# Kernel tuning notes

Hardware: AMD Instinct MI355X
Metric: run time of the kernel (lower is better)

## Reference

```python
import jax, jax.numpy as jnp
import numpy as np
import math

B, T, C = 8, 1024, 64  # n_head = 1 (forced by the module's relative-attention matmul shapes)


def setup_inputs() -> dict:
    key = jax.random.key(0)
    ks = jax.random.split(key, 7)
    x = jax.random.normal(ks[0], (B, T, C), dtype=jnp.float32)
    Wqkv = jax.random.normal(ks[1], (3 * C, C), dtype=jnp.float32) * 0.02
    bqkv = jnp.zeros((3 * C,), dtype=jnp.float32)
    embk = jax.random.normal(ks[2], (T, C), dtype=jnp.float32) * 0.02
    embv = jax.random.normal(ks[3], (T, C), dtype=jnp.float32) * 0.02
    Wproj = jax.random.normal(ks[4], (C, C), dtype=jnp.float32) * 0.02
    bproj = jnp.zeros((C,), dtype=jnp.float32)
    return {"x": x, "Wqkv": Wqkv, "bqkv": bqkv, "embk": embk, "embv": embv,
            "Wproj": Wproj, "bproj": bproj}


def reference(x, Wqkv, bqkv, embk, embv, Wproj, bproj):
    b, t, c = x.shape
    qkv = x @ Wqkv.T + bqkv                      # [B,T,3C]
    q, k, v = jnp.split(qkv, 3, axis=2)          # each [B,T,C]; n_head=1 so head_dim=C

    # relative_pos[i,j] = (i-j).tril() -> 0 above diagonal (masked out anyway)
    idx = jnp.arange(t)
    rel = jnp.tril(idx[:, None] - idx[None, :])  # [T,T] ints in [0, T-1]
    rk = embk[rel]                               # [T,T,C] gathered relative keys
    rv = embv[rel]                               # [T,T,C] gathered relative values

    att1 = jnp.einsum('btc,bsc->bts', q, k)      # content-content scores
    att2 = jnp.einsum('tbc,tsc->bts', q.transpose(1, 0, 2), rk)  # content-position scores
    scale = 1.0 / math.sqrt(c)
    att = (att1 + att2) * scale

    causal = jnp.tril(jnp.ones((t, t), dtype=bool))
    att = jnp.where(causal[None, :, :], att, -jnp.inf)
    att = jax.nn.softmax(att, axis=-1)           # [B,T,T]

    y1 = jnp.einsum('bts,bsc->btc', att, v)      # content values
    y2 = jnp.einsum('bts,tsc->btc', att, rv)     # relative values
    y = y1 + y2                                  # [B,T,C]
    return y @ Wproj.T + bproj
```

## Files before the change

kernel.cpp:

```cpp
#include <hip/hip_runtime.h>
#include <math.h>

#define BB 8
#define TT 1024
#define CC 64

typedef float f32x4 __attribute__((ext_vector_type(4)));
typedef short short8 __attribute__((ext_vector_type(8)));
typedef unsigned int u32x4 __attribute__((ext_vector_type(4)));
typedef unsigned short u16;

static __device__ __forceinline__ u16 f2bf(float f) {
    union { float f; unsigned int u; } v; v.f = f;
    unsigned int r = v.u + 0x7fffu + ((v.u >> 16) & 1u);
    return (u16)(r >> 16);
}
static __device__ __forceinline__ float bf2f(u16 h) {
    union { unsigned int u; float f; } v; v.u = ((unsigned int)h) << 16; return v.f;
}
static __device__ __forceinline__ short8 pack8(const float* p) {
    float4 a = *(const float4*)p;
    float4 b = *(const float4*)(p + 4);
    short8 r;
    r[0] = (short)f2bf(a.x); r[1] = (short)f2bf(a.y); r[2] = (short)f2bf(a.z); r[3] = (short)f2bf(a.w);
    r[4] = (short)f2bf(b.x); r[5] = (short)f2bf(b.y); r[6] = (short)f2bf(b.z); r[7] = (short)f2bf(b.w);
    return r;
}

#define MFMA16(a, b, c) __builtin_amdgcn_mfma_f32_16x16x32_bf16((a), (b), (c), 0, 0, 0)

#define OFF_QBF      ((size_t)0)
#define OFF_KBF      ((size_t)1048576)
#define OFF_VT       ((size_t)2097152)
#define OFF_EKP      ((size_t)3145728)
#define OFF_EVT      ((size_t)3284992)
#define OFF_WPROJ    ((size_t)3424256)
#define OFF_YP       ((size_t)3432448)
#define OFF_LP       ((size_t)20209664)
#define WS_NEED      ((size_t)20471808)

__global__ __launch_bounds__(256) void qkv_prep_kernel(const float* __restrict__ x,
                                                       const float* __restrict__ Wqkv,
                                                       const float* __restrict__ bqkv,
                                                       const float* __restrict__ embk,
                                                       const float* __restrict__ embv,
                                                       const float* __restrict__ Wproj,
                                                       u16* __restrict__ q_bf,
                                                       u16* __restrict__ k_bf,
                                                       u16* __restrict__ vT_bf,
                                                       u16* __restrict__ embk_pad,
                                                       u16* __restrict__ embvT_pad,
                                                       u16* __restrict__ Wproj_bf) {
    const int blk = blockIdx.x;
    const int grp = blockIdx.y;
    const int tid = threadIdx.x;

    if (blk >= 512) {
        if (grp != 0) return;
        const int idx0 = (blk - 512) * 256 + tid;
        const int stride = 64 * 256;
        for (int i = idx0; i < 1088 * CC; i += stride) {
            int r = i >> 6, c = i & 63, d = r - 32;
            embk_pad[i] = (d >= 0 && d < TT) ? f2bf(embk[d * CC + c]) : (u16)0;
        }
        for (int i = idx0; i < CC * 1088; i += stride) {
            int c = i / 1088, col = i - c * 1088, d = col - 32;
            embvT_pad[i] = (d >= 0 && d < TT) ? f2bf(embv[d * CC + c]) : (u16)0;
        }
        for (int i = idx0; i < CC * CC; i += stride) Wproj_bf[i] = f2bf(Wproj[i]);
        return;
    }

    const int w = tid >> 6, lane = tid & 63, quad = lane >> 4, l15 = lane & 15;
    const int row0 = blk * 16;
    const int oc = grp * 4 + w;
    __shared__ float vt[4][16][17];

    const float* xr = x + (size_t)(row0 + l15) * CC + quad * 8;
    short8 a0 = pack8(xr);
    short8 a1 = pack8(xr + 32);

    const float* wr = Wqkv + (size_t)(oc * 16 + l15) * CC + quad * 8;
    short8 b0 = pack8(wr);
    short8 b1 = pack8(wr + 32);
    f32x4 acc = {0.f, 0.f, 0.f, 0.f};
    acc = MFMA16(a0, b0, acc);
    acc = MFMA16(a1, b1, acc);
    const float bias = bqkv[oc * 16 + l15];

    if (oc < 4) {
        const int c = oc * 16 + l15;
        #pragma unroll
        for (int r = 0; r < 4; ++r)
            q_bf[(size_t)(row0 + quad * 4 + r) * CC + c] = f2bf((acc[r] + bias) * 0.125f);
    } else if (oc < 8) {
        const int c = (oc - 4) * 16 + l15;
        #pragma unroll
        for (int r = 0; r < 4; ++r)
            k_bf[(size_t)(row0 + quad * 4 + r) * CC + c] = f2bf(acc[r] + bias);
    } else {
        #pragma unroll
        for (int r = 0; r < 4; ++r) vt[w][quad * 4 + r][l15] = acc[r] + bias;
        const int c_l = lane >> 2;
        const int tbase = (lane & 3) * 4;
        const int b = row0 >> 10, t0v = row0 & (TT - 1);
        u16 p[4];
        #pragma unroll
        for (int tt2 = 0; tt2 < 4; ++tt2) p[tt2] = f2bf(vt[w][tbase + tt2][c_l]);
        unsigned long long pk = (unsigned long long)p[0] | ((unsigned long long)p[1] << 16)
                              | ((unsigned long long)p[2] << 32) | ((unsigned long long)p[3] << 48);
        *(unsigned long long*)&vT_bf[(size_t)(b * CC + (oc - 8) * 16 + c_l) * TT + t0v + tbase] = pk;
    }
}

#define WBSTRIDE 4160

__global__ __launch_bounds__(256) void attn_part_kernel(const u16* __restrict__ q_bf,
                                                        const u16* __restrict__ k_bf,
                                                        const u16* __restrict__ vT_bf,
                                                        const u16* __restrict__ embk_pad,
                                                        const u16* __restrict__ embvT_pad,
                                                        float* __restrict__ Ypart,
                                                        float* __restrict__ Lpart) {
    const int b = blockIdx.y;
    int xx = blockIdx.x;
    int tt = 0, slot = 0;
    for (tt = 0; tt < 64; ++tt) {
        const int c = ((tt >> 1) + 4) >> 2;
        if (xx < c) { slot = xx; break; }
        xx -= c;
    }
    const int t0 = tt * 16;
    const int nst = (t0 >> 5) + 1;

    const int tid = threadIdx.x;
    const int w = tid >> 6, lane = tid & 63, quad = lane >> 4, l15 = lane & 15;
    const int st = slot * 4 + w;
    const bool active = (st < nst);

    __shared__ __align__(16) char wbuf[4][WBSTRIDE];
    __shared__ float lpart[4][16];

    u16* pt = (u16*)(wbuf[w]);
    u16* a2 = (u16*)(wbuf[w] + 1280);

    f32x4 acc[4];
    #pragma unroll
    for (int nb = 0; nb < 4; ++nb) acc[nb] = (f32x4){0.f, 0.f, 0.f, 0.f};
    float rsum[4] = {0.f, 0.f, 0.f, 0.f};

    if (active) {
        const int s0 = st * 32;

        const u16* qrow = q_bf + (size_t)((b << 10) + t0 + l15) * CC;
        short8 aq0 = *(const short8*)(qrow + quad * 8);
        short8 aq1 = *(const short8*)(qrow + 32 + quad * 8);

        f32x4 sc[2];
        #pragma unroll
        for (int cb = 0; cb < 2; ++cb) {
            const u16* krow = k_bf + (size_t)((b << 10) + s0 + cb * 16 + l15) * CC;
            short8 kb0 = *(const short8*)(krow + quad * 8);
            short8 kb1 = *(const short8*)(krow + 32 + quad * 8);
            f32x4 a = {0.f, 0.f, 0.f, 0.f};
            a = MFMA16(aq0, kb0, a);
            a = MFMA16(aq1, kb1, a);
            sc[cb] = a;
        }

        const int dbase = t0 - s0 - 31;
        f32x4 bnd[3];
        #pragma unroll
        for (int nb = 0; nb < 3; ++nb) {
            const u16* erow = embk_pad + (size_t)(dbase + 32 + nb * 16 + l15) * CC;
            short8 eb0 = *(const short8*)(erow + quad * 8);
            short8 eb1 = *(const short8*)(erow + 32 + quad * 8);
            f32x4 a = {0.f, 0.f, 0.f, 0.f};
            a = MFMA16(aq0, eb0, a);
            a = MFMA16(aq1, eb1, a);
            bnd[nb] = a;
        }

        u16 pb0[4], pb1[4];
        #pragma unroll
        for (int r = 0; r < 4; ++r) {
            const int i = quad * 4 + r;
            const int u0 = 31 + i - l15;
            const int src = (quad << 4) | (u0 & 15);
            const float v0 = __shfl(bnd[0][r], src, 64);
            const float v1 = __shfl(bnd[1][r], src, 64);
            const float v2 = __shfl(bnd[2][r], src, 64);
            const bool hi = (u0 >= 32);
            {
                const float rb = hi ? v2 : v1;
                const int d = t0 - s0 + i - l15;
                float pv = (d >= 0) ? __expf(sc[0][r] + rb) : 0.f;
                pb0[r] = f2bf(pv);
                rsum[r] += bf2f(pb0[r]);
            }
            {
                const float rb = hi ? v1 : v0;
                const int d = t0 - s0 + i - 16 - l15;
                float pv = (d >= 0) ? __expf(sc[1][r] + rb) : 0.f;
                pb1[r] = f2bf(pv);
                rsum[r] += bf2f(pb1[r]);
            }
        }

        u32x4 z = {0u, 0u, 0u, 0u};
        #pragma unroll
        for (int e = 0; e < 3; ++e) {
            int idx = lane + e * 64;
            if (idx < 144) ((u32x4*)a2)[idx] = z;
        }
        #pragma unroll
        for (int r = 0; r < 4; ++r) {
            const int i = quad * 4 + r;
            pt[i * 40 + l15] = pb0[r];
            pt[i * 40 + 16 + l15] = pb1[r];
            a2[i * 72 + (32 + i - l15)] = pb0[r];
            a2[i * 72 + (16 + i - l15)] = pb1[r];
        }

        short8 aP = *(const short8*)(pt + l15 * 40 + quad * 8);
        #pragma unroll
        for (int nb = 0; nb < 4; ++nb) {
            const u16* vrow = vT_bf + ((size_t)(b * CC + nb * 16 + l15) << 10) + s0;
            short8 bv = *(const short8*)(vrow + quad * 8);
            acc[nb] = MFMA16(aP, bv, acc[nb]);
        }

        const int dcol0 = t0 - s0;
        #pragma unroll
        for (int kk = 0; kk < 2; ++kk) {
            short8 a2f = *(const short8*)(a2 + l15 * 72 + kk * 32 + quad * 8);
            #pragma unroll
            for (int nb = 0; nb < 4; ++nb) {
                const u16* erow = embvT_pad + (size_t)(nb * 16 + l15) * 1088 + dcol0 + kk * 32 + quad * 8;
                short8 be = *(const short8*)erow;
                acc[nb] = MFMA16(a2f, be, acc[nb]);
            }
        }
    }

    #pragma unroll
    for (int msk = 1; msk < 16; msk <<= 1)
        #pragma unroll
        for (int r = 0; r < 4; ++r) rsum[r] += __shfl_xor(rsum[r], msk, 64);
    if (l15 == 0) {
        #pragma unroll
        for (int r = 0; r < 4; ++r) lpart[w][quad * 4 + r] = rsum[r];
    }

    float* ypw = (float*)(wbuf[w]);
    #pragma unroll
    for (int nb = 0; nb < 4; ++nb)
        #pragma unroll
        for (int r = 0; r < 4; ++r)
            ypw[(quad * 4 + r) * 64 + nb * 16 + l15] = acc[nb][r];
    __syncthreads();

    const size_t sbase = ((size_t)((b * 64 + tt) * 8 + slot)) << 10;
    {
        const int i = tid >> 4, c0 = (tid * 4) & 63;
        float4 Y;
        Y.x = ((float*)(wbuf[0]))[i * 64 + c0]     + ((float*)(wbuf[1]))[i * 64 + c0]
            + ((float*)(wbuf[2]))[i * 64 + c0]     + ((float*)(wbuf[3]))[i * 64 + c0];
        Y.y = ((float*)(wbuf[0]))[i * 64 + c0 + 1] + ((float*)(wbuf[1]))[i * 64 + c0 + 1]
            + ((float*)(wbuf[2]))[i * 64 + c0 + 1] + ((float*)(wbuf[3]))[i * 64 + c0 + 1];
        Y.z = ((float*)(wbuf[0]))[i * 64 + c0 + 2] + ((float*)(wbuf[1]))[i * 64 + c0 + 2]
            + ((float*)(wbuf[2]))[i * 64 + c0 + 2] + ((float*)(wbuf[3]))[i * 64 + c0 + 2];
        Y.w = ((float*)(wbuf[0]))[i * 64 + c0 + 3] + ((float*)(wbuf[1]))[i * 64 + c0 + 3]
            + ((float*)(wbuf[2]))[i * 64 + c0 + 3] + ((float*)(wbuf[3]))[i * 64 + c0 + 3];
        *(float4*)&Ypart[sbase + (size_t)tid * 4] = Y;
    }
    if (tid < 16)
        Lpart[((size_t)((b * 64 + tt) * 8 + slot)) * 16 + tid] =
            lpart[0][tid] + lpart[1][tid] + lpart[2][tid] + lpart[3][tid];
}

__global__ __launch_bounds__(256) void norm_proj_kernel(const float* __restrict__ Ypart,
                                                        const float* __restrict__ Lpart,
                                                        const u16* __restrict__ Wproj_bf,
                                                        const float* __restrict__ bproj,
                                                        float* __restrict__ out) {
    const int b = blockIdx.y;
    const int tt = blockIdx.x;
    const int t0 = tt * 16;
    const int nslots = ((tt >> 1) + 4) >> 2;
    const int tid = threadIdx.x;
    const int w = tid >> 6, lane = tid & 63, quad = lane >> 4, l15 = lane & 15;

    __shared__ float Ls[16];
    __shared__ __align__(16) u16 yA[16 * 64];

    const size_t base = ((size_t)((b * 64 + tt) * 8)) << 10;
    float4 Y = {0.f, 0.f, 0.f, 0.f};
    for (int s = 0; s < nslots; ++s) {
        float4 v = *(const float4*)&Ypart[base + ((size_t)s << 10) + (size_t)tid * 4];
        Y.x += v.x; Y.y += v.y; Y.z += v.z; Y.w += v.w;
    }
    if (tid < 16) {
        float L = 0.f;
        for (int s = 0; s < nslots; ++s)
            L += Lpart[((size_t)((b * 64 + tt) * 8 + s)) * 16 + tid];
        Ls[tid] = L;
    }
    __syncthreads();

    const int i = tid >> 4, c0 = (tid * 4) & 63;
    const float inv = 1.0f / Ls[i];
    u16 y4[4] = { f2bf(Y.x * inv), f2bf(Y.y * inv), f2bf(Y.z * inv), f2bf(Y.w * inv) };
    *(unsigned long long*)&yA[i * 64 + c0] =
        (unsigned long long)y4[0] | ((unsigned long long)y4[1] << 16)
      | ((unsigned long long)y4[2] << 32) | ((unsigned long long)y4[3] << 48);
    __syncthreads();

    short8 a0 = *(const short8*)(yA + l15 * 64 + quad * 8);
    short8 a1 = *(const short8*)(yA + l15 * 64 + 32 + quad * 8);
    const u16* wrow = Wproj_bf + (size_t)(w * 16 + l15) * CC;
    short8 wb0 = *(const short8*)(wrow + quad * 8);
    short8 wb1 = *(const short8*)(wrow + 32 + quad * 8);
    f32x4 o = {0.f, 0.f, 0.f, 0.f};
    o = MFMA16(a0, wb0, o);
    o = MFMA16(a1, wb1, o);
    const float bias = bproj[w * 16 + l15];
    #pragma unroll
    for (int r = 0; r < 4; ++r)
        out[(size_t)((b << 10) + t0 + quad * 4 + r) * CC + w * 16 + l15] = o[r] + bias;
}

__global__ __launch_bounds__(192) void qkv_kernel(const float* __restrict__ x,
                                                  const float* __restrict__ Wqkv,
                                                  const float* __restrict__ bqkv,
                                                  float* __restrict__ qkv) {
    __shared__ __align__(16) float xs[CC];
    const int row = blockIdx.x;
    const int j = threadIdx.x;
    if (j < CC) xs[j] = x[row * CC + j];
    __syncthreads();
    const float* w = Wqkv + j * CC;
    float acc = bqkv[j];
    #pragma unroll
    for (int c = 0; c < CC; c += 4) {
        float4 wq = *(const float4*)(w + c);
        float4 xq = *(const float4*)(xs + c);
        acc += wq.x * xq.x + wq.y * xq.y + wq.z * xq.z + wq.w * xq.w;
    }
    qkv[row * 192 + j] = acc;
}

__global__ __launch_bounds__(256) void attn_kernel(const float* __restrict__ qkv,
                                                   const float* __restrict__ embk,
                                                   const float* __restrict__ embv,
                                                   const float* __restrict__ Wproj,
                                                   const float* __restrict__ bproj,
                                                   float* __restrict__ out) {
    __shared__ __align__(16) float qs[CC];
    __shared__ __align__(16) float sc[TT];
    __shared__ float red[256];
    __shared__ float yred[4][CC];
    const int bt = blockIdx.x;
    const int b = bt >> 10, t = bt & (TT - 1);
    const int tid = threadIdx.x;
    if (tid < CC) qs[tid] = qkv[bt * 192 + tid];
    __syncthreads();
    float lmax = -1e30f;
    for (int s = tid; s <= t; s += 256) {
        const float* krow = qkv + (b * TT + s) * 192 + 64;
        const float* erow = embk + (t - s) * CC;
        float acc = 0.f;
        #pragma unroll
        for (int c = 0; c < CC; c += 4) {
            float4 kq = *(const float4*)(krow + c);
            float4 eq = *(const float4*)(erow + c);
            float4 qq = *(const float4*)(qs + c);
            acc += qq.x * (kq.x + eq.x) + qq.y * (kq.y + eq.y)
                 + qq.z * (kq.z + eq.z) + qq.w * (kq.w + eq.w);
        }
        acc *= 0.125f;
        sc[s] = acc;
        lmax = fmaxf(lmax, acc);
    }
    red[tid] = lmax; __syncthreads();
    for (int off = 128; off > 0; off >>= 1) { if (tid < off) red[tid] = fmaxf(red[tid], red[tid + off]); __syncthreads(); }
    const float m = red[0]; __syncthreads();
    float lsum = 0.f;
    for (int s = tid; s <= t; s += 256) { float e = __expf(sc[s] - m); sc[s] = e; lsum += e; }
    red[tid] = lsum; __syncthreads();
    for (int off = 128; off > 0; off >>= 1) { if (tid < off) red[tid] += red[tid + off]; __syncthreads(); }
    const float inv = 1.0f / red[0]; __syncthreads();
    const int c = tid & 63, g = tid >> 6;
    float acc = 0.f;
    for (int s = g; s <= t; s += 4) {
        float p = sc[s];
        float vv = qkv[(b * TT + s) * 192 + 128 + c];
        float ev = embv[(t - s) * CC + c];
        acc += p * (vv + ev);
    }
    yred[g][c] = acc * inv;
    __syncthreads();
    if (tid < CC) qs[tid] = yred[0][tid] + yred[1][tid] + yred[2][tid] + yred[3][tid];
    __syncthreads();
    if (tid < CC) {
        const float* w = Wproj + tid * CC;
        float o = bproj[tid];
        #pragma unroll
        for (int cc2 = 0; cc2 < CC; cc2 += 4) {
            float4 wq = *(const float4*)(w + cc2);
            float4 yq = *(const float4*)(qs + cc2);
            o += wq.x * yq.x + wq.y * yq.y + wq.z * yq.z + wq.w * yq.w;
        }
        out[bt * CC + tid] = o;
    }
}

extern "C" void kernel_launch(void* const* d_in, const int* in_sizes, int n_in,
                              void* d_out, int out_size, void* d_ws, size_t ws_size,
                              hipStream_t stream) {
    const float* x     = (const float*)d_in[0];
    const float* Wqkv  = (const float*)d_in[1];
    const float* bqkv  = (const float*)d_in[2];
    const float* embk  = (const float*)d_in[3];
    const float* embv  = (const float*)d_in[4];
    const float* Wproj = (const float*)d_in[5];
    const float* bproj = (const float*)d_in[6];
    float* out = (float*)d_out;

    if (ws_size < WS_NEED) {
        float* qkv = (float*)d_ws;
        qkv_kernel<<<BB * TT, 192, 0, stream>>>(x, Wqkv, bqkv, qkv);
        attn_kernel<<<BB * TT, 256, 0, stream>>>(qkv, embk, embv, Wproj, bproj, out);
        return;
    }

    char* ws = (char*)d_ws;
    u16* q_bf       = (u16*)(ws + OFF_QBF);
    u16* k_bf       = (u16*)(ws + OFF_KBF);
    u16* vT_bf      = (u16*)(ws + OFF_VT);
    u16* embk_pad   = (u16*)(ws + OFF_EKP);
    u16* embvT_pad  = (u16*)(ws + OFF_EVT);
    u16* Wproj_bf   = (u16*)(ws + OFF_WPROJ);
    float* Ypart    = (float*)(ws + OFF_YP);
    float* Lpart    = (float*)(ws + OFF_LP);

    qkv_prep_kernel<<<dim3(576, 3), 256, 0, stream>>>(x, Wqkv, bqkv, embk, embv, Wproj,
                                                      q_bf, k_bf, vT_bf, embk_pad, embvT_pad, Wproj_bf);
    attn_part_kernel<<<dim3(288, 8), 256, 0, stream>>>(q_bf, k_bf, vT_bf, embk_pad, embvT_pad,
                                                       Ypart, Lpart);
    norm_proj_kernel<<<dim3(64, 8), 256, 0, stream>>>(Ypart, Lpart, Wproj_bf, bproj, out);
}
```

Baseline: 111.0 us.

## Fuse split-K reduction and output projection into attention kernel via last-block counter

Removes the separate normalize/projection kernel. Each attention block writes its partial result, then bumps a per-tile atomic counter, and the last block to finish reduces all partials and applies the output projection. Tiles with a single slot skip the global partial writes entirely. Counters are zeroed in the prep kernel. This saves one kernel launch and some global traffic, at the cost of threadfences, atomics and a serialized tail on the last block.

New measurement: 419.3 us. +277.8%, slower.

```diff
diff --git a/kernel.cpp b/kernel.cpp
--- a/kernel.cpp
+++ b/kernel.cpp
@@ -37,7 +37,8 @@
 #define OFF_WPROJ    ((size_t)3424256)
 #define OFF_YP       ((size_t)3432448)
 #define OFF_LP       ((size_t)20209664)
-#define WS_NEED      ((size_t)20471808)
+#define OFF_CNT      ((size_t)20471808)
+#define WS_NEED      ((size_t)20473856)
 
 __global__ __launch_bounds__(256) void qkv_prep_kernel(const float* __restrict__ x,
                                                        const float* __restrict__ Wqkv,
@@ -50,12 +51,18 @@
                                                        u16* __restrict__ vT_bf,
                                                        u16* __restrict__ embk_pad,
                                                        u16* __restrict__ embvT_pad,
-                                                       u16* __restrict__ Wproj_bf) {
+                                                       u16* __restrict__ Wproj_bf,
+                                                       int* __restrict__ cnt) {
     const int blk = blockIdx.x;
     const int grp = blockIdx.y;
     const int tid = threadIdx.x;
 
     if (blk >= 512) {
+        if (grp == 1) {
+            const int idx = (blk - 512) * 256 + tid;
+            if (idx < BB * 64) cnt[idx] = 0;
+            return;
+        }
         if (grp != 0) return;
         const int idx0 = (blk - 512) * 256 + tid;
         const int stride = 64 * 256;
@@ -115,13 +122,17 @@
 
 #define WBSTRIDE 4160
 
-__global__ __launch_bounds__(256) void attn_part_kernel(const u16* __restrict__ q_bf,
-                                                        const u16* __restrict__ k_bf,
-                                                        const u16* __restrict__ vT_bf,
-                                                        const u16* __restrict__ embk_pad,
-                                                        const u16* __restrict__ embvT_pad,
-                                                        float* __restrict__ Ypart,
-                                                        float* __restrict__ Lpart) {
+__global__ __launch_bounds__(256) void attn_fused_kernel(const u16* __restrict__ q_bf,
+                                                         const u16* __restrict__ k_bf,
+                                                         const u16* __restrict__ vT_bf,
+                                                         const u16* __restrict__ embk_pad,
+                                                         const u16* __restrict__ embvT_pad,
+                                                         float* __restrict__ Ypart,
+                                                         float* __restrict__ Lpart,
+                                                         const u16* __restrict__ Wproj_bf,
+                                                         const float* __restrict__ bproj,
+                                                         float* __restrict__ out,
+                                                         int* __restrict__ cnt) {
     const int b = blockIdx.y;
     int xx = blockIdx.x;
     int tt = 0, slot = 0;
@@ -132,6 +143,7 @@
     }
     const int t0 = tt * 16;
     const int nst = (t0 >> 5) + 1;
+    const int nslots = ((tt >> 1) + 4) >> 2;
 
     const int tid = threadIdx.x;
     const int w = tid >> 6, lane = tid & 63, quad = lane >> 4, l15 = lane & 15;
@@ -140,6 +152,9 @@
 
     __shared__ __align__(16) char wbuf[4][WBSTRIDE];
     __shared__ float lpart[4][16];
+    __shared__ float Ls[16];
+    __shared__ __align__(16) u16 yA[16 * 64];
+    __shared__ int isLast;
 
     u16* pt = (u16*)(wbuf[w]);
     u16* a2 = (u16*)(wbuf[w] + 1280);
@@ -260,55 +275,52 @@
             ypw[(quad * 4 + r) * 64 + nb * 16 + l15] = acc[nb][r];
     __syncthreads();
 
-    const size_t sbase = ((size_t)((b * 64 + tt) * 8 + slot)) << 10;
-    {
-        const int i = tid >> 4, c0 = (tid * 4) & 63;
-        float4 Y;
-        Y.x = ((float*)(wbuf[0]))[i * 64 + c0]     + ((float*)(wbuf[1]))[i * 64 + c0]
-            + ((float*)(wbuf[2]))[i * 64 + c0]     + ((float*)(wbuf[3]))[i * 64 + c0];
-        Y.y = ((float*)(wbuf[0]))[i * 64 + c0 + 1] + ((float*)(wbuf[1]))[i * 64 + c0 + 1]
-            + ((float*)(wbuf[2]))[i * 64 + c0 + 1] + ((float*)(wbuf[3]))[i * 64 + c0 + 1];
-        Y.z = ((float*)(wbuf[0]))[i * 64 + c0 + 2] + ((float*)(wbuf[1]))[i * 64 + c0 + 2]
-            + ((float*)(wbuf[2]))[i * 64 + c0 + 2] + ((float*)(wbuf[3]))[i * 64 + c0 + 2];
-        Y.w = ((float*)(wbuf[0]))[i * 64 + c0 + 3] + ((float*)(wbuf[1]))[i * 64 + c0 + 3]
-            + ((float*)(wbuf[2]))[i * 64 + c0 + 3] + ((float*)(wbuf[3]))[i * 64 + c0 + 3];
+    const int i = tid >> 4, c0 = (tid * 4) & 63;
+    float4 Y;
+    Y.x = ((float*)(wbuf[0]))[i * 64 + c0]     + ((float*)(wbuf[1]))[i * 64 + c0]
+        + ((float*)(wbuf[2]))[i * 64 + c0]     + ((float*)(wbuf[3]))[i * 64 + c0];
+    Y.y = ((float*)(wbuf[0]))[i * 64 + c0 + 1] + ((float*)(wbuf[1]))[i * 64 + c0 + 1]
+        + ((float*)(wbuf[2]))[i * 64 + c0 + 1] + ((float*)(wbuf[3]))[i * 64 + c0 + 1];
+    Y.z = ((float*)(wbuf[0]))[i * 64 + c0 + 2] + ((float*)(wbuf[1]))[i * 64 + c0 + 2]
+        + ((float*)(wbuf[2]))[i * 64 + c0 + 2] + ((float*)(wbuf[3]))[i * 64 + c0 + 2];
+    Y.w = ((float*)(wbuf[0]))[i * 64 + c0 + 3] + ((float*)(wbuf[1]))[i * 64 + c0 + 3]
+        + ((float*)(wbuf[2]))[i * 64 + c0 + 3] + ((float*)(wbuf[3]))[i * 64 + c0 + 3];
+
+    if (nslots > 1) {
+        const size_t sbase = ((size_t)((b * 64 + tt) * 8 + slot)) << 10;
         *(float4*)&Ypart[sbase + (size_t)tid * 4] = Y;
-    }
-    if (tid < 16)
-        Lpart[((size_t)((b * 64 + tt) * 8 + slot)) * 16 + tid] =
-            lpart[0][tid] + lpart[1][tid] + lpart[2][tid] + lpart[3][tid];
-}
-
-__global__ __launch_bounds__(256) void norm_proj_kernel(const float* __restrict__ Ypart,
-                                                        const float* __restrict__ Lpart,
-                                                        const u16* __restrict__ Wproj_bf,
-                                                        const float* __restrict__ bproj,
-                                                        float* __restrict__ out) {
-    const int b = blockIdx.y;
-    const int tt = blockIdx.x;
-    const int t0 = tt * 16;
-    const int nslots = ((tt >> 1) + 4) >> 2;
-    const int tid = threadIdx.x;
-    const int w = tid >> 6, lane = tid & 63, quad = lane >> 4, l15 = lane & 15;
-
-    __shared__ float Ls[16];
-    __shared__ __align__(16) u16 yA[16 * 64];
-
-    const size_t base = ((size_t)((b * 64 + tt) * 8)) << 10;
-    float4 Y = {0.f, 0.f, 0.f, 0.f};
-    for (int s = 0; s < nslots; ++s) {
-        float4 v = *(const float4*)&Ypart[base + ((size_t)s << 10) + (size_t)tid * 4];
-        Y.x += v.x; Y.y += v.y; Y.z += v.z; Y.w += v.w;
-    }
-    if (tid < 16) {
-        float L = 0.f;
-        for (int s = 0; s < nslots; ++s)
-            L += Lpart[((size_t)((b * 64 + tt) * 8 + s)) * 16 + tid];
-        Ls[tid] = L;
-    }
-    __syncthreads();
-
-    const int i = tid >> 4, c0 = (tid * 4) & 63;
+        if (tid < 16)
+            Lpart[((size_t)((b * 64 + tt) * 8 + slot)) * 16 + tid] =
+                lpart[0][tid] + lpart[1][tid] + lpart[2][tid] + lpart[3][tid];
+        __threadfence();
+        if (tid == 0) {
+            const int old = atomicAdd(&cnt[b * 64 + tt], 1);
+            isLast = (old == nslots - 1);
+        }
+        __syncthreads();
+        if (!isLast) return;
+        __threadfence();
+
+        const size_t base = ((size_t)((b * 64 + tt) * 8)) << 10;
+        for (int s = 0; s < nslots; ++s) {
+            if (s == slot) continue;
+            float4 v = *(const float4*)&Ypart[base + ((size_t)s << 10) + (size_t)tid * 4];
+            Y.x += v.x; Y.y += v.y; Y.z += v.z; Y.w += v.w;
+        }
+        if (tid < 16) {
+            float L = lpart[0][tid] + lpart[1][tid] + lpart[2][tid] + lpart[3][tid];
+            for (int s = 0; s < nslots; ++s) {
+                if (s == slot) continue;
+                L += Lpart[((size_t)((b * 64 + tt) * 8 + s)) * 16 + tid];
+            }
+            Ls[tid] = L;
+        }
+    } else {
+        if (tid < 16)
+            Ls[tid] = lpart[0][tid] + lpart[1][tid] + lpart[2][tid] + lpart[3][tid];
+    }
+    __syncthreads();
+
     const float inv = 1.0f / Ls[i];
     u16 y4[4] = { f2bf(Y.x * inv), f2bf(Y.y * inv), f2bf(Y.z * inv), f2bf(Y.w * inv) };
     *(unsigned long long*)&yA[i * 64 + c0] =
@@ -443,10 +455,11 @@
     u16* Wproj_bf   = (u16*)(ws + OFF_WPROJ);
     float* Ypart    = (float*)(ws + OFF_YP);
     float* Lpart    = (float*)(ws + OFF_LP);
+    int*   cnt      = (int*)(ws + OFF_CNT);
 
     qkv_prep_kernel<<<dim3(576, 3), 256, 0, stream>>>(x, Wqkv, bqkv, embk, embv, Wproj,
-                                                      q_bf, k_bf, vT_bf, embk_pad, embvT_pad, Wproj_bf);
-    attn_part_kernel<<<dim3(288, 8), 256, 0, stream>>>(q_bf, k_bf, vT_bf, embk_pad, embvT_pad,
-                                                       Ypart, Lpart);
-    norm_proj_kernel<<<dim3(64, 8), 256, 0, stream>>>(Ypart, Lpart, Wproj_bf, bproj, out);
-}
+                                                      q_bf, k_bf, vT_bf, embk_pad, embvT_pad,
+                                                      Wproj_bf, cnt);
+    attn_fused_kernel<<<dim3(288, 8), 256, 0, stream>>>(q_bf, k_bf, vT_bf, embk_pad, embvT_pad,
+                                                        Ypart, Lpart, Wproj_bf, bproj, out, cnt);
+}
```

## Fuse attention partials with normalization and projection in one looping kernel

Applied to the files above, without the earlier changes.

The split-KV attention kernel, which wrote per-slot partial sums to global workspace, and the separate norm/projection kernel are merged into one kernel. Each 512-thread block handles one 16-row query tile, with 8 waves looping over key strips, reducing in shared memory, then normalizing and projecting directly to the output. The grid is reversed so the longest causal tiles start first. This removes the Ypart/Lpart global round trip and one kernel launch, at the cost of fewer blocks (512 versus 2304) and longer serial loops for late tiles, which may reduce parallelism.

Measured after the change: 118.5 us. 6.7% more time.

```diff
diff --git a/kernel.cpp b/kernel.cpp
--- a/kernel.cpp
+++ b/kernel.cpp
@@ -35,9 +35,7 @@
 #define OFF_EKP      ((size_t)3145728)
 #define OFF_EVT      ((size_t)3284992)
 #define OFF_WPROJ    ((size_t)3424256)
-#define OFF_YP       ((size_t)3432448)
-#define OFF_LP       ((size_t)20209664)
-#define WS_NEED      ((size_t)20471808)
+#define WS_NEED      ((size_t)3432448)
 
 __global__ __launch_bounds__(256) void qkv_prep_kernel(const float* __restrict__ x,
                                                        const float* __restrict__ Wqkv,
@@ -115,31 +113,26 @@
 
 #define WBSTRIDE 4160
 
-__global__ __launch_bounds__(256) void attn_part_kernel(const u16* __restrict__ q_bf,
+__global__ __launch_bounds__(512) void attn_loop_kernel(const u16* __restrict__ q_bf,
                                                         const u16* __restrict__ k_bf,
                                                         const u16* __restrict__ vT_bf,
                                                         const u16* __restrict__ embk_pad,
                                                         const u16* __restrict__ embvT_pad,
-                                                        float* __restrict__ Ypart,
-                                                        float* __restrict__ Lpart) {
+                                                        const u16* __restrict__ Wproj_bf,
+                                                        const float* __restrict__ bproj,
+                                                        float* __restrict__ out) {
     const int b = blockIdx.y;
-    int xx = blockIdx.x;
-    int tt = 0, slot = 0;
-    for (tt = 0; tt < 64; ++tt) {
-        const int c = ((tt >> 1) + 4) >> 2;
-        if (xx < c) { slot = xx; break; }
-        xx -= c;
-    }
+    const int tt = 63 - blockIdx.x;
     const int t0 = tt * 16;
     const int nst = (t0 >> 5) + 1;
 
     const int tid = threadIdx.x;
     const int w = tid >> 6, lane = tid & 63, quad = lane >> 4, l15 = lane & 15;
-    const int st = slot * 4 + w;
-    const bool active = (st < nst);
-
-    __shared__ __align__(16) char wbuf[4][WBSTRIDE];
-    __shared__ float lpart[4][16];
+
+    __shared__ __align__(16) char wbuf[8][WBSTRIDE];
+    __shared__ float lpart[8][16];
+    __shared__ float Ls[16];
+    __shared__ __align__(16) u16 yA[16 * 64];
 
     u16* pt = (u16*)(wbuf[w]);
     u16* a2 = (u16*)(wbuf[w] + 1280);
@@ -149,12 +142,12 @@
     for (int nb = 0; nb < 4; ++nb) acc[nb] = (f32x4){0.f, 0.f, 0.f, 0.f};
     float rsum[4] = {0.f, 0.f, 0.f, 0.f};
 
-    if (active) {
+    const u16* qrow = q_bf + (size_t)((b << 10) + t0 + l15) * CC;
+    short8 aq0 = *(const short8*)(qrow + quad * 8);
+    short8 aq1 = *(const short8*)(qrow + 32 + quad * 8);
+
+    for (int st = w; st < nst; st += 8) {
         const int s0 = st * 32;
-
-        const u16* qrow = q_bf + (size_t)((b << 10) + t0 + l15) * CC;
-        short8 aq0 = *(const short8*)(qrow + quad * 8);
-        short8 aq1 = *(const short8*)(qrow + 32 + quad * 8);
 
         f32x4 sc[2];
         #pragma unroll
@@ -260,74 +253,49 @@
             ypw[(quad * 4 + r) * 64 + nb * 16 + l15] = acc[nb][r];
     __syncthreads();
 
-    const size_t sbase = ((size_t)((b * 64 + tt) * 8 + slot)) << 10;
-    {
-        const int i = tid >> 4, c0 = (tid * 4) & 63;
-        float4 Y;
-        Y.x = ((float*)(wbuf[0]))[i * 64 + c0]     + ((float*)(wbuf[1]))[i * 64 + c0]
-            + ((float*)(wbuf[2]))[i * 64 + c0]     + ((float*)(wbuf[3]))[i * 64 + c0];
-        Y.y = ((float*)(wbuf[0]))[i * 64 + c0 + 1] + ((float*)(wbuf[1]))[i * 64 + c0 + 1]
-            + ((float*)(wbuf[2]))[i * 64 + c0 + 1] + ((float*)(wbuf[3]))[i * 64 + c0 + 1];
-        Y.z = ((float*)(wbuf[0]))[i * 64 + c0 + 2] + ((float*)(wbuf[1]))[i * 64 + c0 + 2]
-            + ((float*)(wbuf[2]))[i * 64 + c0 + 2] + ((float*)(wbuf[3]))[i * 64 + c0 + 2];
-        Y.w = ((float*)(wbuf[0]))[i * 64 + c0 + 3] + ((float*)(wbuf[1]))[i * 64 + c0 + 3]
-            + ((float*)(wbuf[2]))[i * 64 + c0 + 3] + ((float*)(wbuf[3]))[i * 64 + c0 + 3];
-        *(float4*)&Ypart[sbase + (size_t)tid * 4] = Y;
-    }
-    if (tid < 16)
-        Lpart[((size_t)((b * 64 + tt) * 8 + slot)) * 16 + tid] =
-            lpart[0][tid] + lpart[1][tid] + lpart[2][tid] + lpart[3][tid];
-}
-
-__global__ __launch_bounds__(256) void norm_proj_kernel(const float* __restrict__ Ypart,
-                                                        const float* __restrict__ Lpart,
-                                                        const u16* __restrict__ Wproj_bf,
-                                                        const float* __restrict__ bproj,
-                                                        float* __restrict__ out) {
-    const int b = blockIdx.y;
-    const int tt = blockIdx.x;
-    const int t0 = tt * 16;
-    const int nslots = ((tt >> 1) + 4) >> 2;
-    const int tid = threadIdx.x;
-    const int w = tid >> 6, lane = tid & 63, quad = lane >> 4, l15 = lane & 15;
-
-    __shared__ float Ls[16];
-    __shared__ __align__(16) u16 yA[16 * 64];
-
-    const size_t base = ((size_t)((b * 64 + tt) * 8)) << 10;
+    const int i = tid >> 4, c0 = (tid * 4) & 63;
     float4 Y = {0.f, 0.f, 0.f, 0.f};
-    for (int s = 0; s < nslots; ++s) {
-        float4 v = *(const float4*)&Ypart[base + ((size_t)s << 10) + (size_t)tid * 4];
-        Y.x += v.x; Y.y += v.y; Y.z += v.z; Y.w += v.w;
-    }
-    if (tid < 16) {
-        float L = 0.f;
-        for (int s = 0; s < nslots; ++s)
-            L += Lpart[((size_t)((b * 64 + tt) * 8 + s)) * 16 + tid];
-        Ls[tid] = L;
-    }
-    __syncthreads();
-
-    const int i = tid >> 4, c0 = (tid * 4) & 63;
-    const float inv = 1.0f / Ls[i];
-    u16 y4[4] = { f2bf(Y.x * inv), f2bf(Y.y * inv), f2bf(Y.z * inv), f2bf(Y.w * inv) };
-    *(unsigned long long*)&yA[i * 64 + c0] =
-        (unsigned long long)y4[0] | ((unsigned long long)y4[1] << 16)
-      | ((unsigned long long)y4[2] << 32) | ((unsigned long long)y4[3] << 48);
-    __syncthreads();
-
-    short8 a0 = *(const short8*)(yA + l15 * 64 + quad * 8);
-    short8 a1 = *(const short8*)(yA + l15 * 64 + 32 + quad * 8);
-    const u16* wrow = Wproj_bf + (size_t)(w * 16 + l15) * CC;
-    short8 wb0 = *(const short8*)(wrow + quad * 8);
-    short8 wb1 = *(const short8*)(wrow + 32 + quad * 8);
-    f32x4 o = {0.f, 0.f, 0.f, 0.f};
-    o = MFMA16(a0, wb0, o);
-    o = MFMA16(a1, wb1, o);
-    const float bias = bproj[w * 16 + l15];
-    #pragma unroll
-    for (int r = 0; r < 4; ++r)
-        out[(size_t)((b << 10) + t0 + quad * 4 + r) * CC + w * 16 + l15] = o[r] + bias;
+    if (tid < 256) {
+        #pragma unroll
+        for (int ww = 0; ww < 8; ++ww) {
+            const float* src = (const float*)(wbuf[ww]);
+            Y.x += src[i * 64 + c0];
+            Y.y += src[i * 64 + c0 + 1];
+            Y.z += src[i * 64 + c0 + 2];
+            Y.w += src[i * 64 + c0 + 3];
+        }
+        if (tid < 16) {
+            float L = 0.f;
+            #pragma unroll
+            for (int ww = 0; ww < 8; ++ww) L += lpart[ww][tid];
+            Ls[tid] = L;
+        }
+    }
+    __syncthreads();
+
+    if (tid < 256) {
+        const float inv = 1.0f / Ls[i];
+        u16 y4[4] = { f2bf(Y.x * inv), f2bf(Y.y * inv), f2bf(Y.z * inv), f2bf(Y.w * inv) };
+        *(unsigned long long*)&yA[i * 64 + c0] =
+            (unsigned long long)y4[0] | ((unsigned long long)y4[1] << 16)
+          | ((unsigned long long)y4[2] << 32) | ((unsigned long long)y4[3] << 48);
+    }
+    __syncthreads();
+
+    if (w < 4) {
+        short8 a0 = *(const short8*)(yA + l15 * 64 + quad * 8);
+        short8 a1 = *(const short8*)(yA + l15 * 64 + 32 + quad * 8);
+        const u16* wrow = Wproj_bf + (size_t)(w * 16 + l15) * CC;
+        short8 wb0 = *(const short8*)(wrow + quad * 8);
+        short8 wb1 = *(const short8*)(wrow + 32 + quad * 8);
+        f32x4 o = {0.f, 0.f, 0.f, 0.f};
+        o = MFMA16(a0, wb0, o);
+        o = MFMA16(a1, wb1, o);
+        const float bias = bproj[w * 16 + l15];
+        #pragma unroll
+        for (int r = 0; r < 4; ++r)
+            out[(size_t)((b << 10) + t0 + quad * 4 + r) * CC + w * 16 + l15] = o[r] + bias;
+    }
 }
 
 __global__ __launch_bounds__(192) void qkv_kernel(const float* __restrict__ x,
@@ -441,12 +409,9 @@
     u16* embk_pad   = (u16*)(ws + OFF_EKP);
     u16* embvT_pad  = (u16*)(ws + OFF_EVT);
     u16* Wproj_bf   = (u16*)(ws + OFF_WPROJ);
-    float* Ypart    = (float*)(ws + OFF_YP);
-    float* Lpart    = (float*)(ws + OFF_LP);
 
     qkv_prep_kernel<<<dim3(576, 3), 256, 0, stream>>>(x, Wqkv, bqkv, embk, embv, Wproj,
                                                       q_bf, k_bf, vT_bf, embk_pad, embvT_pad, Wproj_bf);
-    attn_part_kernel<<<dim3(288, 8), 256, 0, stream>>>(q_bf, k_bf, vT_bf, embk_pad, embvT_pad,
-                                                       Ypart, Lpart);
-    norm_proj_kernel<<<dim3(64, 8), 256, 0, stream>>>(Ypart, Lpart, Wproj_bf, bproj, out);
-}
+    attn_loop_kernel<<<dim3(64, 8), 512, 0, stream>>>(q_bf, k_bf, vT_bf, embk_pad, embvT_pad,
+                                                      Wproj_bf, bproj, out);
+}
```
